# Kernel tuning notes

Measured on AMD Instinct MI355X. Metric: run time of the kernel, lower is better.

The kernel has to match this reference:

```python
import jax, jax.numpy as jnp
import numpy as np

EPS = 1e-5  # nn.BatchNorm2d default eps


def _cbs(x, w, g, b, m, v):
    # Conv(k=1, bias=False) + BatchNorm2d(inference) + SiLU
    y = jnp.einsum('bchw,oc->bohw', x, w)
    s = (g * jax.lax.rsqrt(v + EPS))[None, :, None, None]
    y = (y - m[None, :, None, None]) * s + b[None, :, None, None]
    return y * jax.nn.sigmoid(y)


def setup_inputs():
    key = jax.random.key(0)
    B, D, H, W = 1, 256, 80, 80
    C = D // 2
    ks = jax.random.split(key, 20)
    r = lambda i, shape, sc=1.0: jax.random.normal(ks[i], shape, dtype=jnp.float32) * sc
    oC, oD = jnp.ones((C,), jnp.float32), jnp.ones((D,), jnp.float32)
    zC, zD = jnp.zeros((C,), jnp.float32), jnp.zeros((D,), jnp.float32)
    return {
        'x': r(0, (B, D, H, W)),
        'w1': r(1, (C, D), 0.05), 'g1': oC, 'b1': zC, 'm1': zC, 'v1': oC,
        'w2': r(2, (D, C), 0.05), 'g2': oD, 'b2': zD, 'm2': zD, 'v2': oD,
        'w3': r(3, (D, C), 0.05), 'g3': oD, 'b3': zD, 'm3': zD, 'v3': oD,
        'wq': r(4, (C, C), 0.05), 'bq': r(5, (C,), 0.01),
        'wk': r(6, (C, C), 0.05), 'bk': r(7, (C,), 0.01),
        'wv': r(8, (C, C), 0.05), 'bv': r(9, (C,), 0.01),
        'wp': r(10, (C, C), 0.05), 'bp': r(11, (C,), 0.01),
        'rel_h': r(12, (1, C, H, 1)), 'rel_w': r(13, (1, C, 1, W)),
        'ef_h': r(14, (1, C, H, 1)), 'ef_w': r(15, (1, C, 1, W)),
    }


def reference(x, w1, g1, b1, m1, v1, w2, g2, b2, m2, v2, w3, g3, b3, m3, v3,
              wq, bq, wk, bk, wv, bv, wp, bp, rel_h, rel_w, ef_h, ef_w):
    x1 = _cbs(x, w1, g1, b1, m1, v1)            # [B, C, H, W]
    B, C, H, W = x1.shape
    HW = H * W
    proj = lambda w, b: (jnp.einsum('bchw,oc->bohw', x1, w)
                         + b[None, :, None, None]).reshape(B, C, HW)
    q = proj(wq, bq)
    k = proj(wk, bk)
    v = proj(wv, bv)
    p = proj(wp, bp)
    # content-content + content-position attention branch
    cp = (rel_h + rel_w).reshape(C, HW)          # [C, HW]
    cc = jnp.einsum('bci,bcj->bij', q, k)        # [B, HW, HW]
    cpos = jnp.einsum('ci,bcj->bij', cp, q)      # [B, HW, HW]
    attn = jax.nn.softmax(cc + cpos, axis=-1)
    # out1[b,c,i] = sum_j v[b,c,j] * attn[b,i,j]  (bmm(v, attn^T))
    out1 = jnp.einsum('bcj,bij->bci', v, attn).reshape(B, C, H, W)
    # extra positional branch (valid because B == 1)
    ef = (ef_h + ef_w).reshape(B, C, HW)         # [1, C, HW]
    ce = jnp.einsum('bci,bcj->bij', p, ef)       # [B, HW, HW]
    eng = jax.nn.softmax(ce, axis=-1)
    out2 = jnp.einsum('bcj,bij->bci', ef, eng).reshape(B, C, H, W)
    return x + _cbs(out1, w2, g2, b2, m2, v2) + _cbs(out2, w3, g3, b3, m3, v3)
```

## Files before the change

### kernel.cpp

```cpp
#include <hip/hip_runtime.h>


typedef unsigned short u16;
typedef __attribute__((ext_vector_type(8))) short bf16x8;
typedef __attribute__((ext_vector_type(4))) float f32x4;
typedef __attribute__((ext_vector_type(4))) unsigned int u32x4;

#define HW 6400
#define BN_EPS 1e-5f

__device__ __forceinline__ u16 f2b(float f) {
  unsigned u = __float_as_uint(f);
  u += 0x7fffu + ((u >> 16) & 1u);
  return (u16)(u >> 16);
}
__device__ __forceinline__ unsigned pack2(float a, float b) {
  return (unsigned)f2b(a) | ((unsigned)f2b(b) << 16);
}
__device__ __forceinline__ f32x4 MFMA(bf16x8 a, bf16x8 b, f32x4 c) {
  return __builtin_amdgcn_mfma_f32_16x16x32_bf16(a, b, c, 0, 0, 0);
}
__device__ __forceinline__ float silu_f(float y) {
  return y / (1.0f + __expf(-y));
}
__device__ __forceinline__ bf16x8 pack8(f32x4 lo, f32x4 hi, float sc) {
  union { bf16x8 v; uint4 u; } r;
  r.u.x = pack2(lo[0] * sc, lo[1] * sc);
  r.u.y = pack2(lo[2] * sc, lo[3] * sc);
  r.u.z = pack2(hi[0] * sc, hi[1] * sc);
  r.u.w = pack2(hi[2] * sc, hi[3] * sc);
  return r.v;
}
__device__ __forceinline__ void gload_lds16(const u16* src, u16* dst) {
  __builtin_amdgcn_global_load_lds(
      (const __attribute__((address_space(1))) void*)src,
      (__attribute__((address_space(3))) void*)dst, 16, 0, 0);
}

__global__ void prep_all(
    const float* __restrict__ rel_h, const float* __restrict__ rel_w,
    const float* __restrict__ ef_h, const float* __restrict__ ef_w,
    const float* __restrict__ w1, const float* __restrict__ g1, const float* __restrict__ b1,
    const float* __restrict__ m1, const float* __restrict__ v1,
    const float* __restrict__ w2, const float* __restrict__ g2, const float* __restrict__ b2,
    const float* __restrict__ m2, const float* __restrict__ v2,
    const float* __restrict__ w3, const float* __restrict__ g3, const float* __restrict__ b3,
    const float* __restrict__ m3, const float* __restrict__ v3,
    const float* __restrict__ wq, const float* __restrict__ bq,
    const float* __restrict__ wk, const float* __restrict__ bk,
    const float* __restrict__ wv, const float* __restrict__ bv,
    const float* __restrict__ wp, const float* __restrict__ bp,
    u16* __restrict__ LT,
    u16* __restrict__ w1b, float* __restrict__ b1e,
    u16* __restrict__ Wcat, float* __restrict__ bcat,
    u16* __restrict__ w2b, float* __restrict__ b2e,
    u16* __restrict__ w3b, float* __restrict__ b3e,
    u16* __restrict__ efhT, u16* __restrict__ efwT,
    u16* __restrict__ efhB, u16* __restrict__ efwB,
    u16* __restrict__ expA, u16* __restrict__ expB,
    float* __restrict__ lbuf)
{
  const int b = blockIdx.x;
  const int t = threadIdx.x;
  if (b < 80) {
    const int h = b;
    const int c0 = (t & 63) * 2;
    const float rh0 = rel_h[c0 * 80 + h], rh1 = rel_h[(c0 + 1) * 80 + h];
    for (int wcol = (t >> 6); wcol < 80; wcol += 4) {
      const int i = h * 80 + wcol;
      float rw0 = rel_w[c0 * 80 + wcol], rw1 = rel_w[(c0 + 1) * 80 + wcol];
      *(unsigned*)&LT[(size_t)i * 256 + 128 + c0] = pack2(rh0 + rw0, rh1 + rw1);
    }
  } else if (b < 144) {
    const int tid = (b - 80) * 256 + t;
    const int stride = 64 * 256;
    for (int idx = tid; idx < 128 * 256; idx += stride) {
      int o = idx >> 8;
      float s = g1[o] * rsqrtf(v1[o] + BN_EPS);
      w1b[idx] = f2b(w1[idx] * s);
    }
    for (int idx = tid; idx < 128; idx += stride) {
      float s = g1[idx] * rsqrtf(v1[idx] + BN_EPS);
      b1e[idx] = b1[idx] - m1[idx] * s;
    }
    for (int idx = tid; idx < 4 * 128 * 128; idx += stride) {
      int which = idx >> 14, r = idx & 16383;
      const float* src = which == 0 ? wq : which == 1 ? wk : which == 2 ? wv : wp;
      Wcat[idx] = f2b(src[r]);
    }
    for (int idx = tid; idx < 512; idx += stride) {
      int which = idx >> 7, r = idx & 127;
      const float* src = which == 0 ? bq : which == 1 ? bk : which == 2 ? bv : bp;
      bcat[idx] = src[r];
    }
    for (int idx = tid; idx < 256 * 128; idx += stride) {
      int o = idx >> 7;
      float s2 = g2[o] * rsqrtf(v2[o] + BN_EPS);
      w2b[idx] = f2b(w2[idx] * s2);
      float s3 = g3[o] * rsqrtf(v3[o] + BN_EPS);
      w3b[idx] = f2b(w3[idx] * s3);
    }
    for (int idx = tid; idx < 256; idx += stride) {
      float s2 = g2[idx] * rsqrtf(v2[idx] + BN_EPS);
      b2e[idx] = b2[idx] - m2[idx] * s2;
      float s3 = g3[idx] * rsqrtf(v3[idx] + BN_EPS);
      b3e[idx] = b3[idx] - m3[idx] * s3;
    }
    for (int idx = tid; idx < 80 * 128; idx += stride) {
      int hj = idx >> 7, c = idx & 127;
      efhT[idx] = f2b(ef_h[c * 80 + hj]);
      efwT[idx] = f2b(ef_w[c * 80 + hj]);
    }
    for (int idx = tid; idx < 128 * 96; idx += stride) {
      int c = idx / 96, hj = idx % 96;
      efhB[idx] = hj < 80 ? f2b(ef_h[c * 80 + hj]) : (u16)0;
      efwB[idx] = hj < 80 ? f2b(ef_w[c * 80 + hj]) : (u16)0;
    }
  } else {
    const int tid = (b - 144) * 256 + t;
    const int stride = 32 * 256;
    for (int idx = tid; idx < HW / 4; idx += stride)
      ((f32x4*)lbuf)[idx] = (f32x4){0.f, 0.f, 0.f, 0.f};
    for (int idx = tid; idx < HW * 96 / 8; idx += stride) {
      ((u32x4*)expA)[idx] = (u32x4){0, 0, 0, 0};
      ((u32x4*)expB)[idx] = (u32x4){0, 0, 0, 0};
    }
  }
}

__global__ __launch_bounds__(64) void front_k(
    const float* __restrict__ x,
    const u16* __restrict__ w1b, const float* __restrict__ b1e,
    const u16* __restrict__ Wcat, const float* __restrict__ bcat,
    u16* __restrict__ LT, u16* __restrict__ RT, u16* __restrict__ Vv,
    u16* __restrict__ pT)
{
  __shared__ __align__(16) float xs[16][260];
  __shared__ __align__(16) u16 tr[16][136];
  const int t = threadIdx.x, lane = t & 63, jl = lane & 15, q = lane >> 4;
  const int i0 = blockIdx.x * 16;

#pragma unroll
  for (int p = 0; p < 16; ++p) {
    const int ch = p * 16 + (lane >> 2);
    const int ii = (lane & 3) * 4;
    f32x4 v = *(const f32x4*)(x + (size_t)ch * HW + i0 + ii);
    xs[ii][ch] = v[0]; xs[ii + 1][ch] = v[1];
    xs[ii + 2][ch] = v[2]; xs[ii + 3][ch] = v[3];
  }
  __syncthreads();

  bf16x8 afr[8];
#pragma unroll
  for (int ks = 0; ks < 8; ++ks) {
    f32x4 va = *(const f32x4*)&xs[jl][ks * 32 + q * 8];
    f32x4 vb = *(const f32x4*)&xs[jl][ks * 32 + q * 8 + 4];
    afr[ks] = pack8(va, vb, 1.0f);
  }
  f32x4 acc[8];
#pragma unroll
  for (int nf = 0; nf < 8; ++nf) acc[nf] = (f32x4){0.f, 0.f, 0.f, 0.f};
#pragma unroll
  for (int ks = 0; ks < 8; ++ks)
#pragma unroll
    for (int nf = 0; nf < 8; ++nf) {
      bf16x8 b = *(const bf16x8*)(w1b + (size_t)(nf * 16 + jl) * 256 + ks * 32 + q * 8);
      acc[nf] = MFMA(afr[ks], b, acc[nf]);
    }
#pragma unroll
  for (int nf = 0; nf < 8; ++nf) {
    const int c = nf * 16 + jl;
    const float bias = b1e[c];
#pragma unroll
    for (int r = 0; r < 4; ++r)
      tr[q * 4 + r][c] = f2b(silu_f(acc[nf][r] + bias));
  }
  __syncthreads();
  bf16x8 xa[4];
#pragma unroll
  for (int ks = 0; ks < 4; ++ks)
    xa[ks] = *(const bf16x8*)&tr[jl][ks * 32 + q * 8];

#pragma unroll
  for (int nc = 0; nc < 4; ++nc) {
    f32x4 a2[8];
#pragma unroll
    for (int nf = 0; nf < 8; ++nf) a2[nf] = (f32x4){0.f, 0.f, 0.f, 0.f};
#pragma unroll
    for (int ks = 0; ks < 4; ++ks)
#pragma unroll
      for (int nf = 0; nf < 8; ++nf) {
        bf16x8 b = *(const bf16x8*)(Wcat + (size_t)(nc * 128 + nf * 16 + jl) * 128 + ks * 32 + q * 8);
        a2[nf] = MFMA(xa[ks], b, a2[nf]);
      }
    if (nc == 2) {
#pragma unroll
      for (int nf = 0; nf < 8; ++nf) {
        const int c = nf * 16 + jl;
        const float bias = bcat[256 + c];
        uint2 pk;
        pk.x = pack2(a2[nf][0] + bias, a2[nf][1] + bias);
        pk.y = pack2(a2[nf][2] + bias, a2[nf][3] + bias);
        *(uint2*)(Vv + (size_t)c * HW + i0 + q * 4) = pk;
      }
    } else {
      __syncthreads();
#pragma unroll
      for (int nf = 0; nf < 8; ++nf) {
        const int c = nf * 16 + jl;
        const float bias = bcat[nc * 128 + c];
#pragma unroll
        for (int r = 0; r < 4; ++r)
          tr[q * 4 + r][c] = f2b(a2[nf][r] + bias);
      }
      __syncthreads();
#pragma unroll
      for (int r = 0; r < 16; ++r) {
        unsigned val = *(const unsigned*)&tr[r][lane * 2];
        const size_t row = (size_t)(i0 + r);
        if (nc == 0) {
          *(unsigned*)(LT + row * 256 + lane * 2) = val;
          *(unsigned*)(RT + row * 256 + 128 + lane * 2) = val;
        } else if (nc == 1) {
          *(unsigned*)(RT + row * 256 + lane * 2) = val;
        } else {
          *(unsigned*)(pT + row * 128 + lane * 2) = val;
        }
      }
    }
  }
}

__device__ __forceinline__ void sep2a_body(
    int b2,
    const u16* __restrict__ pT, const u16* __restrict__ efhT,
    const u16* __restrict__ efwT,
    u16* __restrict__ expA, u16* __restrict__ expB,
    float* __restrict__ sA, float* __restrict__ sB)
{
  const int t = threadIdx.x, lane = t & 63, w = t >> 6, jl = lane & 15, q = lane >> 4;
  const int i0w = b2 * 256 + w * 32;

  bf16x8 pfr[2][4];
#pragma unroll
  for (int mt = 0; mt < 2; ++mt)
#pragma unroll
    for (int l = 0; l < 4; ++l)
      pfr[mt][l] = *(const bf16x8*)(pT + (size_t)(i0w + mt * 16 + jl) * 128 + l * 32 + q * 8);

  f32x4 sa[5][2], sb[5][2];
#pragma unroll
  for (int nf = 0; nf < 5; ++nf)
#pragma unroll
    for (int mt = 0; mt < 2; ++mt) {
      sa[nf][mt] = (f32x4){0.f, 0.f, 0.f, 0.f};
      sb[nf][mt] = (f32x4){0.f, 0.f, 0.f, 0.f};
    }
#pragma unroll
  for (int nf = 0; nf < 5; ++nf) {
    const int row = nf * 16 + jl;
#pragma unroll
    for (int l = 0; l < 4; ++l) {
      bf16x8 eh = *(const bf16x8*)(efhT + (size_t)row * 128 + l * 32 + q * 8);
      bf16x8 ew = *(const bf16x8*)(efwT + (size_t)row * 128 + l * 32 + q * 8);
      sa[nf][0] = MFMA(eh, pfr[0][l], sa[nf][0]);
      sa[nf][1] = MFMA(eh, pfr[1][l], sa[nf][1]);
      sb[nf][0] = MFMA(ew, pfr[0][l], sb[nf][0]);
      sb[nf][1] = MFMA(ew, pfr[1][l], sb[nf][1]);
    }
  }
#pragma unroll
  for (int mt = 0; mt < 2; ++mt) {
    const int i = i0w + mt * 16 + jl;
    float ra = 0.f, rb = 0.f;
#pragma unroll
    for (int nf = 0; nf < 5; ++nf) {
      float ea[4], eb[4];
#pragma unroll
      for (int r = 0; r < 4; ++r) {
        ea[r] = __expf(sa[nf][mt][r]); ra += ea[r];
        eb[r] = __expf(sb[nf][mt][r]); rb += eb[r];
      }
      uint2 pa, pb;
      pa.x = pack2(ea[0], ea[1]); pa.y = pack2(ea[2], ea[3]);
      pb.x = pack2(eb[0], eb[1]); pb.y = pack2(eb[2], eb[3]);
      *(uint2*)(expA + (size_t)i * 96 + nf * 16 + q * 4) = pa;
      *(uint2*)(expB + (size_t)i * 96 + nf * 16 + q * 4) = pb;
    }
    ra += __shfl_xor(ra, 16); ra += __shfl_xor(ra, 32);
    rb += __shfl_xor(rb, 16); rb += __shfl_xor(rb, 32);
    if (lane < 16) { sA[i] = ra; sB[i] = rb; }
  }
}

__global__ __launch_bounds__(512, 2) void fused_attn(
    const u16* __restrict__ LT,
    const u16* __restrict__ RT,
    const u16* __restrict__ Vv,
    float* __restrict__ Opart,
    float* __restrict__ lv,
    const u16* __restrict__ pT, const u16* __restrict__ efhT,
    const u16* __restrict__ efwT,
    u16* __restrict__ expA, u16* __restrict__ expB,
    float* __restrict__ sA, float* __restrict__ sB)
{
  __shared__ __align__(1024) u16 Rs[2][128 * 128];
  __shared__ __align__(1024) u16 Ts[2][64 * 128];
  const int bid = blockIdx.x;
  if (bid >= 500) {
    sep2a_body(bid - 500, pT, efhT, efwT, expA, expB, sA, sB);
    return;
  }
  const int t = threadIdx.x, lane = t & 63, w = t >> 6, jl = lane & 15, q = lane >> 4;
  const int it = bid / 10, jp = bid % 10;
  const int wi = w & 1, wj = w >> 1;
  const int i0w = it * 128 + wi * 64;
  u16* Tw = Ts[wi];

  bf16x8 afr[4][8];
#pragma unroll
  for (int mt = 0; mt < 4; ++mt)
#pragma unroll
    for (int l = 0; l < 8; ++l)
      afr[mt][l] = *(const bf16x8*)(LT + (size_t)(i0w + mt * 16 + jl) * 256 + l * 32 + q * 8);

  f32x4 o[4][2];
#pragma unroll
  for (int mt = 0; mt < 4; ++mt)
#pragma unroll
    for (int cf = 0; cf < 2; ++cf) o[mt][cf] = (f32x4){0.f, 0.f, 0.f, 0.f};
  float lacc[4] = {0.f, 0.f, 0.f, 0.f};

  auto stage = [&](int jj) {
#pragma unroll
    for (int k = 0; k < 8; ++k) {
      const int b = k >> 2, cl = k & 3;
      const int cc = w * 4 + cl;
      const int jr = cc * 4 + (lane >> 4);
      const int cp = lane & 15;
      const int ch = (cp & ~7) | ((cp ^ jr) & 7);
      gload_lds16(RT + (size_t)(jj + jr) * 256 + b * 128 + ch * 8,
                  Rs[b] + (cc << 9));
    }
  };

  stage(jp * 640);

  for (int stp = 0; stp < 5; ++stp) {
    const int jj = jp * 640 + stp * 128;

    f32x4 s[2][4];
#pragma unroll
    for (int nf = 0; nf < 2; ++nf)
#pragma unroll
      for (int mt = 0; mt < 4; ++mt) s[nf][mt] = (f32x4){0.f, 0.f, 0.f, 0.f};

    __syncthreads();

#pragma unroll
    for (int h = 0; h < 2; ++h)
#pragma unroll
      for (int nf = 0; nf < 2; ++nf) {
        const int row = wj * 32 + nf * 16 + jl;
#pragma unroll
        for (int l = 0; l < 4; ++l) {
          const int ch = (l * 4 + q) ^ (jl & 7);
          bf16x8 b = *(const bf16x8*)(Rs[h] + row * 128 + ch * 8);
          s[nf][0] = MFMA(b, afr[0][h * 4 + l], s[nf][0]);
          s[nf][1] = MFMA(b, afr[1][h * 4 + l], s[nf][1]);
          s[nf][2] = MFMA(b, afr[2][h * 4 + l], s[nf][2]);
          s[nf][3] = MFMA(b, afr[3][h * 4 + l], s[nf][3]);
        }
      }
    __syncthreads();
    if (stp < 4) stage(jj + 128);

#pragma unroll
    for (int nf = 0; nf < 2; ++nf)
#pragma unroll
      for (int mt = 0; mt < 4; ++mt)
#pragma unroll
        for (int r = 0; r < 4; ++r) {
          float p = __expf(s[nf][mt][r]);
          s[nf][mt][r] = p;
          lacc[mt] += p;
        }

#pragma unroll
    for (int mt = 0; mt < 4; ++mt)
#pragma unroll
      for (int nf = 0; nf < 2; ++nf) {
        const int row = mt * 16 + jl;
        const int cs = (wj * 8 + nf * 4 + q) ^ ((jl & 7) << 2);
        uint2 pk;
        pk.x = pack2(s[nf][mt][0], s[nf][mt][1]);
        pk.y = pack2(s[nf][mt][2], s[nf][mt][3]);
        *(uint2*)(Tw + row * 128 + cs * 4) = pk;
      }
    __syncthreads();

#pragma unroll
    for (int ks2 = 0; ks2 < 4; ++ks2) {
      bf16x8 bv0 = *(const bf16x8*)(Vv + (size_t)(wj * 32 + jl) * HW + jj + ks2 * 32 + q * 8);
      bf16x8 bv1 = *(const bf16x8*)(Vv + (size_t)(wj * 32 + 16 + jl) * HW + jj + ks2 * 32 + q * 8);
      const int cb = (ks2 * 8 + q * 2) ^ ((jl & 7) << 2);
#pragma unroll
      for (int mt = 0; mt < 4; ++mt) {
        bf16x8 pa = *(const bf16x8*)(Tw + (mt * 16 + jl) * 128 + cb * 4);
        o[mt][0] = MFMA(pa, bv0, o[mt][0]);
        o[mt][1] = MFMA(pa, bv1, o[mt][1]);
      }
    }
  }

#pragma unroll
  for (int mt = 0; mt < 4; ++mt) {
    float rsum = lacc[mt];
    rsum += __shfl_xor(rsum, 16);
    rsum += __shfl_xor(rsum, 32);
    if (lane < 16)
      atomicAdd(&lv[i0w + mt * 16 + jl], rsum);
  }
#pragma unroll
  for (int mt = 0; mt < 4; ++mt) {
    const int ib = i0w + mt * 16 + q * 4;
#pragma unroll
    for (int cf = 0; cf < 2; ++cf) {
      const int c = wj * 32 + cf * 16 + jl;
#pragma unroll
      for (int r = 0; r < 4; ++r)
        Opart[((size_t)(ib + r) * 10 + jp) * 128 + c] = o[mt][cf][r];
    }
  }
}

__global__ __launch_bounds__(256) void final2(
    const u16* __restrict__ expA, const u16* __restrict__ expB,
    const float* __restrict__ sA, const float* __restrict__ sB,
    const u16* __restrict__ efhB, const u16* __restrict__ efwB,
    const float* __restrict__ Opart,
    const float* __restrict__ lv,
    const u16* __restrict__ w2b, const float* __restrict__ b2e,
    const u16* __restrict__ w3b, const float* __restrict__ b3e,
    const float* __restrict__ x, float* __restrict__ outp)
{
  __shared__ __align__(16) u16 T2[64][136];
  const int t = threadIdx.x, lane = t & 63, w = t >> 6, jl = lane & 15, q = lane >> 4;
  const int i0 = blockIdx.x * 64;
  const int nc = blockIdx.y;
  const int rowA = i0 + w * 16 + jl;

  {
    bf16x8 fa[3], fb[3];
#pragma unroll
    for (int l = 0; l < 3; ++l) {
      fa[l] = *(const bf16x8*)(expA + (size_t)rowA * 96 + l * 32 + q * 8);
      fb[l] = *(const bf16x8*)(expB + (size_t)rowA * 96 + l * 32 + q * 8);
    }
    f32x4 oU[8], oW[8];
#pragma unroll
    for (int nf = 0; nf < 8; ++nf) {
      oU[nf] = (f32x4){0.f, 0.f, 0.f, 0.f};
      oW[nf] = (f32x4){0.f, 0.f, 0.f, 0.f};
    }
#pragma unroll
    for (int l = 0; l < 3; ++l)
#pragma unroll
      for (int nf = 0; nf < 8; ++nf) {
        bf16x8 bh = *(const bf16x8*)(efhB + (size_t)(nf * 16 + jl) * 96 + l * 32 + q * 8);
        bf16x8 bw = *(const bf16x8*)(efwB + (size_t)(nf * 16 + jl) * 96 + l * 32 + q * 8);
        oU[nf] = MFMA(fa[l], bh, oU[nf]);
        oW[nf] = MFMA(fb[l], bw, oW[nf]);
      }
    const int ib = i0 + w * 16 + q * 4;
    float ia[4], iw[4];
#pragma unroll
    for (int r = 0; r < 4; ++r) {
      ia[r] = 1.0f / sA[ib + r];
      iw[r] = 1.0f / sB[ib + r];
    }
#pragma unroll
    for (int nf = 0; nf < 8; ++nf)
#pragma unroll
      for (int r = 0; r < 4; ++r)
        T2[w * 16 + q * 4 + r][nf * 16 + jl] =
            f2b(oU[nf][r] * ia[r] + oW[nf][r] * iw[r]);
  }
  __syncthreads();

  const float inv1 = 1.0f / lv[rowA];
  const float* OrBase = Opart + (size_t)rowA * 10 * 128;
  f32x4 a1[8], a2[8];
#pragma unroll
  for (int nf = 0; nf < 8; ++nf) {
    a1[nf] = (f32x4){0.f, 0.f, 0.f, 0.f};
    a2[nf] = (f32x4){0.f, 0.f, 0.f, 0.f};
  }
#pragma unroll
  for (int ks = 0; ks < 4; ++ks) {
    f32x4 s1a = (f32x4){0.f, 0.f, 0.f, 0.f};
    f32x4 s1b = (f32x4){0.f, 0.f, 0.f, 0.f};
#pragma unroll
    for (int p = 0; p < 10; ++p) {
      const float* Or = OrBase + p * 128;
      s1a += *(const f32x4*)(Or + ks * 32 + q * 8);
      s1b += *(const f32x4*)(Or + ks * 32 + q * 8 + 4);
    }
    bf16x8 fa1 = pack8(s1a, s1b, inv1);
    bf16x8 fa2 = *(const bf16x8*)&T2[w * 16 + jl][ks * 32 + q * 8];
#pragma unroll
    for (int nf = 0; nf < 8; ++nf) {
      bf16x8 b2f = *(const bf16x8*)(w2b + (size_t)(nc * 128 + nf * 16 + jl) * 128 + ks * 32 + q * 8);
      bf16x8 b3f = *(const bf16x8*)(w3b + (size_t)(nc * 128 + nf * 16 + jl) * 128 + ks * 32 + q * 8);
      a1[nf] = MFMA(fa1, b2f, a1[nf]);
      a2[nf] = MFMA(fa2, b3f, a2[nf]);
    }
  }
#pragma unroll
  for (int nf = 0; nf < 8; ++nf) {
    const int d = nc * 128 + nf * 16 + jl;
    const float bb2 = b2e[d], bb3 = b3e[d];
    const size_t base = (size_t)d * HW + i0 + w * 16 + q * 4;
    f32x4 xv = *(const f32x4*)(x + base);
    f32x4 rv;
#pragma unroll
    for (int r = 0; r < 4; ++r)
      rv[r] = xv[r] + silu_f(a1[nf][r] + bb2) + silu_f(a2[nf][r] + bb3);
    *(f32x4*)(outp + base) = rv;
  }
}

extern "C" void kernel_launch(void* const* d_in, const int* in_sizes, int n_in,
                              void* d_out, int out_size, void* d_ws, size_t ws_size,
                              hipStream_t stream)
{
  (void)in_sizes; (void)n_in; (void)out_size; (void)ws_size;
  const float* x   = (const float*)d_in[0];
  const float* w1  = (const float*)d_in[1];
  const float* g1  = (const float*)d_in[2];
  const float* b1  = (const float*)d_in[3];
  const float* m1  = (const float*)d_in[4];
  const float* v1  = (const float*)d_in[5];
  const float* w2  = (const float*)d_in[6];
  const float* g2  = (const float*)d_in[7];
  const float* b2  = (const float*)d_in[8];
  const float* m2  = (const float*)d_in[9];
  const float* v2  = (const float*)d_in[10];
  const float* w3  = (const float*)d_in[11];
  const float* g3  = (const float*)d_in[12];
  const float* b3  = (const float*)d_in[13];
  const float* m3  = (const float*)d_in[14];
  const float* v3  = (const float*)d_in[15];
  const float* wq  = (const float*)d_in[16];
  const float* bq  = (const float*)d_in[17];
  const float* wk  = (const float*)d_in[18];
  const float* bk  = (const float*)d_in[19];
  const float* wv  = (const float*)d_in[20];
  const float* bv  = (const float*)d_in[21];
  const float* wp  = (const float*)d_in[22];
  const float* bp  = (const float*)d_in[23];
  const float* rel_h = (const float*)d_in[24];
  const float* rel_w = (const float*)d_in[25];
  const float* ef_h  = (const float*)d_in[26];
  const float* ef_w  = (const float*)d_in[27];
  float* outp = (float*)d_out;

  char* ws = (char*)d_ws;
  size_t off = 0;
  auto alloc = [&](size_t bytes) -> void* {
    void* p = ws + off;
    off += (bytes + 511) & ~(size_t)511;
    return p;
  };
  u16* LT    = (u16*)alloc((size_t)HW * 256 * 2);
  u16* RT    = (u16*)alloc((size_t)HW * 256 * 2);
  u16* pT    = (u16*)alloc((size_t)HW * 128 * 2);
  u16* Vv    = (u16*)alloc((size_t)HW * 128 * 2);
  float* Opart = (float*)alloc((size_t)HW * 10 * 128 * 4);
  float* lbuf  = (float*)alloc((size_t)HW * 4);
  u16* w1b   = (u16*)alloc(128 * 256 * 2);
  float* b1e = (float*)alloc(128 * 4);
  u16* Wcat  = (u16*)alloc(512 * 128 * 2);
  float* bcat = (float*)alloc(512 * 4);
  u16* w2b   = (u16*)alloc(256 * 128 * 2);
  float* b2e = (float*)alloc(256 * 4);
  u16* w3b   = (u16*)alloc(256 * 128 * 2);
  float* b3e = (float*)alloc(256 * 4);
  u16* efhT  = (u16*)alloc(80 * 128 * 2);
  u16* efwT  = (u16*)alloc(80 * 128 * 2);
  u16* efhB  = (u16*)alloc(128 * 96 * 2);
  u16* efwB  = (u16*)alloc(128 * 96 * 2);
  u16* expA  = (u16*)alloc((size_t)HW * 96 * 2);
  u16* expB  = (u16*)alloc((size_t)HW * 96 * 2);
  float* sA  = (float*)alloc(HW * 4);
  float* sB  = (float*)alloc(HW * 4);

  prep_all<<<176, 256, 0, stream>>>(rel_h, rel_w, ef_h, ef_w,
                                    w1, g1, b1, m1, v1, w2, g2, b2, m2, v2,
                                    w3, g3, b3, m3, v3, wq, bq, wk, bk, wv, bv, wp, bp,
                                    LT, w1b, b1e, Wcat, bcat, w2b, b2e, w3b, b3e,
                                    efhT, efwT, efhB, efwB, expA, expB, lbuf);
  front_k<<<400, 64, 0, stream>>>(x, w1b, b1e, Wcat, bcat, LT, RT, Vv, pT);
  fused_attn<<<525, 512, 0, stream>>>(LT, RT, Vv, Opart, lbuf,
                                      pT, efhT, efwT, expA, expB, sA, sB);
  final2<<<dim3(100, 2), 256, 0, stream>>>(expA, expB, sA, sB, efhB, efwB,
                                           Opart, lbuf, w2b, b2e, w3b, b3e,
                                           x, outp);
}
```

Baseline: 250.9 us.

## Use 1024-thread attention blocks and split sep2a into its own kernel

Result: slower. 278.0 us (+10.8%).

```diff
diff --git a/kernel.cpp b/kernel.cpp
--- a/kernel.cpp
+++ b/kernel.cpp
@@ -231,15 +231,15 @@
   }
 }
 
-__device__ __forceinline__ void sep2a_body(
-    int b2,
-    const u16* __restrict__ pT, const u16* __restrict__ efhT,
+__global__ __launch_bounds__(256) void sep2a(
+    const u16* __restrict__ pT,
+    const u16* __restrict__ efhT,
     const u16* __restrict__ efwT,
     u16* __restrict__ expA, u16* __restrict__ expB,
     float* __restrict__ sA, float* __restrict__ sB)
 {
   const int t = threadIdx.x, lane = t & 63, w = t >> 6, jl = lane & 15, q = lane >> 4;
-  const int i0w = b2 * 256 + w * 32;
+  const int i0w = blockIdx.x * 128 + w * 32;
 
   bf16x8 pfr[2][4];
 #pragma unroll
@@ -293,54 +293,45 @@
   }
 }
 
-__global__ __launch_bounds__(512, 2) void fused_attn(
+__global__ __launch_bounds__(1024, 4) void fused_attn(
     const u16* __restrict__ LT,
     const u16* __restrict__ RT,
     const u16* __restrict__ Vv,
     float* __restrict__ Opart,
-    float* __restrict__ lv,
-    const u16* __restrict__ pT, const u16* __restrict__ efhT,
-    const u16* __restrict__ efwT,
-    u16* __restrict__ expA, u16* __restrict__ expB,
-    float* __restrict__ sA, float* __restrict__ sB)
+    float* __restrict__ lv)
 {
   __shared__ __align__(1024) u16 Rs[2][128 * 128];
-  __shared__ __align__(1024) u16 Ts[2][64 * 128];
+  __shared__ __align__(1024) u16 Tb[128 * 128];
+  const int t = threadIdx.x, lane = t & 63, w = t >> 6, jl = lane & 15, q = lane >> 4;
   const int bid = blockIdx.x;
-  if (bid >= 500) {
-    sep2a_body(bid - 500, pT, efhT, efwT, expA, expB, sA, sB);
-    return;
-  }
-  const int t = threadIdx.x, lane = t & 63, w = t >> 6, jl = lane & 15, q = lane >> 4;
   const int it = bid / 10, jp = bid % 10;
-  const int wi = w & 1, wj = w >> 1;
-  const int i0w = it * 128 + wi * 64;
-  u16* Tw = Ts[wi];
-
-  bf16x8 afr[4][8];
-#pragma unroll
-  for (int mt = 0; mt < 4; ++mt)
+  const int wi = w & 3, wj = w >> 2;
+  const int i0w = it * 128 + wi * 32;
+
+  bf16x8 afr[2][8];
+#pragma unroll
+  for (int mt = 0; mt < 2; ++mt)
 #pragma unroll
     for (int l = 0; l < 8; ++l)
       afr[mt][l] = *(const bf16x8*)(LT + (size_t)(i0w + mt * 16 + jl) * 256 + l * 32 + q * 8);
 
-  f32x4 o[4][2];
-#pragma unroll
-  for (int mt = 0; mt < 4; ++mt)
+  f32x4 o[2][2];
+#pragma unroll
+  for (int mt = 0; mt < 2; ++mt)
 #pragma unroll
     for (int cf = 0; cf < 2; ++cf) o[mt][cf] = (f32x4){0.f, 0.f, 0.f, 0.f};
-  float lacc[4] = {0.f, 0.f, 0.f, 0.f};
+  float lacc[2] = {0.f, 0.f};
 
   auto stage = [&](int jj) {
 #pragma unroll
-    for (int k = 0; k < 8; ++k) {
-      const int b = k >> 2, cl = k & 3;
-      const int cc = w * 4 + cl;
+    for (int k = 0; k < 4; ++k) {
+      const int bh = k >> 1, cl = k & 1;
+      const int cc = w * 2 + cl;
       const int jr = cc * 4 + (lane >> 4);
       const int cp = lane & 15;
       const int ch = (cp & ~7) | ((cp ^ jr) & 7);
-      gload_lds16(RT + (size_t)(jj + jr) * 256 + b * 128 + ch * 8,
-                  Rs[b] + (cc << 9));
+      gload_lds16(RT + (size_t)(jj + jr) * 256 + bh * 128 + ch * 8,
+                  Rs[bh] + (cc << 9));
     }
   };
 
@@ -349,11 +340,11 @@
   for (int stp = 0; stp < 5; ++stp) {
     const int jj = jp * 640 + stp * 128;
 
-    f32x4 s[2][4];
+    f32x4 s[2][2];
 #pragma unroll
     for (int nf = 0; nf < 2; ++nf)
 #pragma unroll
-      for (int mt = 0; mt < 4; ++mt) s[nf][mt] = (f32x4){0.f, 0.f, 0.f, 0.f};
+      for (int mt = 0; mt < 2; ++mt) s[nf][mt] = (f32x4){0.f, 0.f, 0.f, 0.f};
 
     __syncthreads();
 
@@ -368,8 +359,6 @@
           bf16x8 b = *(const bf16x8*)(Rs[h] + row * 128 + ch * 8);
           s[nf][0] = MFMA(b, afr[0][h * 4 + l], s[nf][0]);
           s[nf][1] = MFMA(b, afr[1][h * 4 + l], s[nf][1]);
-          s[nf][2] = MFMA(b, afr[2][h * 4 + l], s[nf][2]);
-          s[nf][3] = MFMA(b, afr[3][h * 4 + l], s[nf][3]);
         }
       }
     __syncthreads();
@@ -378,7 +367,7 @@
 #pragma unroll
     for (int nf = 0; nf < 2; ++nf)
 #pragma unroll
-      for (int mt = 0; mt < 4; ++mt)
+      for (int mt = 0; mt < 2; ++mt)
 #pragma unroll
         for (int r = 0; r < 4; ++r) {
           float p = __expf(s[nf][mt][r]);
@@ -387,34 +376,34 @@
         }
 
 #pragma unroll
-    for (int mt = 0; mt < 4; ++mt)
+    for (int mt = 0; mt < 2; ++mt)
 #pragma unroll
       for (int nf = 0; nf < 2; ++nf) {
-        const int row = mt * 16 + jl;
+        const int row = wi * 32 + mt * 16 + jl;
         const int cs = (wj * 8 + nf * 4 + q) ^ ((jl & 7) << 2);
         uint2 pk;
         pk.x = pack2(s[nf][mt][0], s[nf][mt][1]);
         pk.y = pack2(s[nf][mt][2], s[nf][mt][3]);
-        *(uint2*)(Tw + row * 128 + cs * 4) = pk;
+        *(uint2*)(Tb + row * 128 + cs * 4) = pk;
       }
     __syncthreads();
 
 #pragma unroll
     for (int ks2 = 0; ks2 < 4; ++ks2) {
-      bf16x8 bv0 = *(const bf16x8*)(Vv + (size_t)(wj * 32 + jl) * HW + jj + ks2 * 32 + q * 8);
-      bf16x8 bv1 = *(const bf16x8*)(Vv + (size_t)(wj * 32 + 16 + jl) * HW + jj + ks2 * 32 + q * 8);
       const int cb = (ks2 * 8 + q * 2) ^ ((jl & 7) << 2);
-#pragma unroll
-      for (int mt = 0; mt < 4; ++mt) {
-        bf16x8 pa = *(const bf16x8*)(Tw + (mt * 16 + jl) * 128 + cb * 4);
-        o[mt][0] = MFMA(pa, bv0, o[mt][0]);
-        o[mt][1] = MFMA(pa, bv1, o[mt][1]);
-      }
-    }
-  }
-
-#pragma unroll
-  for (int mt = 0; mt < 4; ++mt) {
+      bf16x8 pa0 = *(const bf16x8*)(Tb + (wi * 32 + jl) * 128 + cb * 4);
+      bf16x8 pa1 = *(const bf16x8*)(Tb + (wi * 32 + 16 + jl) * 128 + cb * 4);
+#pragma unroll
+      for (int cf = 0; cf < 2; ++cf) {
+        bf16x8 bv = *(const bf16x8*)(Vv + (size_t)(wj * 32 + cf * 16 + jl) * HW + jj + ks2 * 32 + q * 8);
+        o[0][cf] = MFMA(pa0, bv, o[0][cf]);
+        o[1][cf] = MFMA(pa1, bv, o[1][cf]);
+      }
+    }
+  }
+
+#pragma unroll
+  for (int mt = 0; mt < 2; ++mt) {
     float rsum = lacc[mt];
     rsum += __shfl_xor(rsum, 16);
     rsum += __shfl_xor(rsum, 32);
@@ -422,7 +411,7 @@
       atomicAdd(&lv[i0w + mt * 16 + jl], rsum);
   }
 #pragma unroll
-  for (int mt = 0; mt < 4; ++mt) {
+  for (int mt = 0; mt < 2; ++mt) {
     const int ib = i0w + mt * 16 + q * 4;
 #pragma unroll
     for (int cf = 0; cf < 2; ++cf) {
@@ -601,8 +590,8 @@
                                     LT, w1b, b1e, Wcat, bcat, w2b, b2e, w3b, b3e,
                                     efhT, efwT, efhB, efwB, expA, expB, lbuf);
   front_k<<<400, 64, 0, stream>>>(x, w1b, b1e, Wcat, bcat, LT, RT, Vv, pT);
-  fused_attn<<<525, 512, 0, stream>>>(LT, RT, Vv, Opart, lbuf,
-                                      pT, efhT, efwT, expA, expB, sA, sB);
+  sep2a<<<50, 256, 0, stream>>>(pT, efhT, efwT, expA, expB, sA, sB);
+  fused_attn<<<500, 1024, 0, stream>>>(LT, RT, Vv, Opart, lbuf);
   final2<<<dim3(100, 2), 256, 0, stream>>>(expA, expB, sA, sB, efhB, efwB,
                                            Opart, lbuf, w2b, b2e, w3b, b3e,
                                            x, outp);
```
